# Kernel tuning notes

Measured on AMD Instinct MI355X. Metric: run time of the kernel, lower is better.

## Reference

```python
import jax, jax.numpy as jnp
import numpy as np

INPUT_SIZE = 8
HIDDEN = 12
N_ACTIONS = 4
B, T = 4096, 1024


def setup_inputs() -> dict:
    key = jax.random.key(0)
    ks = jax.random.split(key, 7)
    s_ih = 1.0 / np.sqrt(HIDDEN)
    # PyTorch LSTM params: W_ih [4H, I], W_hh [4H, H], b_ih [4H], b_hh [4H]; gate order i,f,g,o
    return {
        "x": jax.random.normal(ks[0], (B, T, INPUT_SIZE), dtype=jnp.float32),
        "W_ih": jax.random.uniform(ks[1], (4 * HIDDEN, INPUT_SIZE), jnp.float32, -s_ih, s_ih),
        "W_hh": jax.random.uniform(ks[2], (4 * HIDDEN, HIDDEN), jnp.float32, -s_ih, s_ih),
        "b_ih": jax.random.uniform(ks[3], (4 * HIDDEN,), jnp.float32, -s_ih, s_ih),
        "b_hh": jax.random.uniform(ks[4], (4 * HIDDEN,), jnp.float32, -s_ih, s_ih),
        "W_fc": jax.random.uniform(ks[5], (N_ACTIONS, HIDDEN), jnp.float32, -s_ih, s_ih),
        "b_fc": jax.random.uniform(ks[6], (N_ACTIONS,), jnp.float32, -s_ih, s_ih),
    }


def _lstm(x, W_ih, W_hh, b_ih, b_hh):
    # x: [B, T, I]. Precompute input contribution for all timesteps (one big GEMM).
    xW = jnp.einsum("bti,gi->tbg", x, W_ih) + (b_ih + b_hh)  # [T, B, 4H]
    Bsz = x.shape[0]
    h0 = jnp.zeros((Bsz, HIDDEN), x.dtype)
    c0 = jnp.zeros((Bsz, HIDDEN), x.dtype)

    def step(carry, xw_t):
        h, c = carry
        gates = xw_t + h @ W_hh.T  # [B, 4H]
        i, f, g, o = jnp.split(gates, 4, axis=-1)  # PyTorch gate order i,f,g,o
        i = jax.nn.sigmoid(i)
        f = jax.nn.sigmoid(f)
        g = jnp.tanh(g)
        o = jax.nn.sigmoid(o)
        c = f * c + i * g
        h = o * jnp.tanh(c)
        return (h, c), h

    (hn, cn), hs = jax.lax.scan(step, (h0, c0), xW)
    return jnp.swapaxes(hs, 0, 1), hn, cn  # hs -> [B, T, H]


def reference(x, W_ih, W_hh, b_ih, b_hh, W_fc, b_fc):
    hs, hn, cn = _lstm(x, W_ih, W_hh, b_ih, b_hh)
    out = hs @ W_fc.T + b_fc  # [B, T, n_actions]
    # match torch: hn/cn have leading num_layers dim (=1)
    return out, (hn[None], cn[None])
```

## Files before the change

### kernel.cpp

```cpp
#include <hip/hip_runtime.h>
#include <cstddef>
#include <cstdint>

namespace {

typedef __fp16 h2v __attribute__((ext_vector_type(2)));

constexpr int kB = 4096, kT = 1024, kI = 8, kH = 12, kA = 4;
constexpr int kTC = 32;
constexpr int kNCH = kT / kTC;
constexpr int kWaveU = 256;
constexpr int kBlkU  = 4 * kWaveU;

constexpr float kL2E  = 1.442695041f;
constexpr float kL2E2 = 2.885390082f;

template<int N>
__device__ __forceinline__ uint32_t ror16u(uint32_t v) {
    return (uint32_t)__builtin_amdgcn_mov_dpp((int)v, 0x120 + N, 0xF, 0xF, false);
}
__device__ __forceinline__ float ror16f1(float v) {
    return __int_as_float(__builtin_amdgcn_mov_dpp(__float_as_int(v), 0x121, 0xF, 0xF, false));
}
__device__ __forceinline__ float bperm(int byte_addr, float v) {
    return __int_as_float(__builtin_amdgcn_ds_bpermute(byte_addr, __float_as_int(v)));
}
__device__ __forceinline__ uint32_t pkrtz(float lo, float hi) {
    auto v = __builtin_amdgcn_cvt_pkrtz(lo, hi);
    return __builtin_bit_cast(uint32_t, v);
}
__device__ __forceinline__ h2v uh(uint32_t u) { return __builtin_bit_cast(h2v, u); }

__global__ __launch_bounds__(256, 2)
void lstm_fused_kernel(const float* __restrict__ x,
                       const float* __restrict__ W_ih,
                       const float* __restrict__ W_hh,
                       const float* __restrict__ b_ih,
                       const float* __restrict__ b_hh,
                       const float* __restrict__ W_fc,
                       const float* __restrict__ b_fc,
                       float* __restrict__ out) {
    __shared__ uint32_t xs[2][kBlkU];

    const int tid = threadIdx.x;
    const int wv  = tid >> 6;
    const int l64 = tid & 63;
    const int ri  = l64 >> 4;
    const int r   = l64 & 15;
    const int e   = ri & 1;
    const int gh  = ri >> 1;
    const int b0  = blockIdx.x * 8 + wv * 2;
    const int b   = b0 + e;
    const bool isFC = (gh == 0) && (r >= kH);
    const int a  = isFC ? (r - kH) : 0;

    const int probe = __builtin_amdgcn_mov_dpp(r, 0x121, 0xF, 0xF, false);
    const int dir   = (probe - r) & 15;

    h2v w1p[8], w2p[8], x1p[4], x2p[4];
    float b1, b2;
    if (r < kH) {
        const int row1 = (gh == 0) ? r : (2 * kH + r);
        const int row2 = (gh == 0) ? (kH + r) : (3 * kH + r);
        const float scl1 = (gh == 0) ? -kL2E : -kL2E2;
        const float scl2 = -kL2E;
#pragma unroll
        for (int j = 0; j < 8; ++j) {
            const int c0 = (r + dir * 2 * j) & 15;
            const int cc = (c0 + dir) & 15;
            const float u0 = (c0 < kH) ? W_hh[row1 * kH + c0] : 0.0f;
            const float u1 = (cc < kH) ? W_hh[row1 * kH + cc] : 0.0f;
            const float v0 = (c0 < kH) ? W_hh[row2 * kH + c0] : 0.0f;
            const float v1 = (cc < kH) ? W_hh[row2 * kH + cc] : 0.0f;
            w1p[j] = h2v{(__fp16)(scl1 * u0), (__fp16)(scl1 * u1)};
            w2p[j] = h2v{(__fp16)(scl2 * v0), (__fp16)(scl2 * v1)};
        }
#pragma unroll
        for (int i2 = 0; i2 < 4; ++i2) {
            x1p[i2] = h2v{(__fp16)(scl1 * W_ih[row1 * kI + 2 * i2]),
                          (__fp16)(scl1 * W_ih[row1 * kI + 2 * i2 + 1])};
            x2p[i2] = h2v{(__fp16)(scl2 * W_ih[row2 * kI + 2 * i2]),
                          (__fp16)(scl2 * W_ih[row2 * kI + 2 * i2 + 1])};
        }
        b1 = scl1 * (b_ih[row1] + b_hh[row1]);
        b2 = scl2 * (b_ih[row2] + b_hh[row2]);
    } else if (gh == 0) {
#pragma unroll
        for (int j = 0; j < 8; ++j) {
            const int c0 = (r + dir * 2 * j) & 15;
            const int cc = (c0 + dir) & 15;
            const float u0 = (c0 < kH) ? W_fc[a * kH + c0] : 0.0f;
            const float u1 = (cc < kH) ? W_fc[a * kH + cc] : 0.0f;
            w1p[j] = h2v{(__fp16)u0, (__fp16)u1};
            w2p[j] = h2v{(__fp16)0.f, (__fp16)0.f};
        }
#pragma unroll
        for (int i2 = 0; i2 < 4; ++i2) {
            x1p[i2] = h2v{(__fp16)0.f, (__fp16)0.f};
            x2p[i2] = h2v{(__fp16)0.f, (__fp16)0.f};
        }
        b1 = b_fc[a]; b2 = 0.0f;
    } else {
#pragma unroll
        for (int j = 0; j < 8; ++j) { w1p[j] = h2v{(__fp16)0.f, (__fp16)0.f}; w2p[j] = w1p[j]; }
#pragma unroll
        for (int i2 = 0; i2 < 4; ++i2) { x1p[i2] = h2v{(__fp16)0.f, (__fp16)0.f}; x2p[i2] = x1p[i2]; }
        b1 = 0.0f; b2 = 0.0f;
    }
    const float m1  = (gh == 0) ? 1.0f : 2.0f;
    const float a1c = (gh == 0) ? 0.0f : -1.0f;
    const int  exa  = (l64 ^ 32) << 2;

    const float* xga = x + (size_t)b0 * (kT * kI);
    const float* xgb = xga + (size_t)kT * kI;
    const int wbu = wv * kWaveU;
    const int rbu = wbu + e * 128;

    float4 rva = ((const float4*)xga)[l64];
    float4 rvb = ((const float4*)xgb)[l64];
    {
        uint2 ua; ua.x = pkrtz(rva.x, rva.y); ua.y = pkrtz(rva.z, rva.w);
        uint2 ub; ub.x = pkrtz(rvb.x, rvb.y); ub.y = pkrtz(rvb.z, rvb.w);
        *(uint2*)&xs[0][wbu + l64 * 2]       = ua;
        *(uint2*)&xs[0][wbu + 128 + l64 * 2] = ub;
    }
    asm volatile("s_waitcnt lgkmcnt(0)" ::: "memory");
    __builtin_amdgcn_sched_barrier(0);
    uint4 xr = *(const uint4*)&xs[0][rbu];

    float h = 0.0f, c = 0.0f;
    uint32_t hrp[8];
#pragma unroll
    for (int k = 0; k < 8; ++k) hrp[k] = 0u;

    float* op = out + (size_t)b * (kT * kA) + a;

    int cb = 0;
#pragma unroll 1
    for (int ch = 0; ch < kNCH; ++ch) {
        if (ch + 1 < kNCH) {
            rva = ((const float4*)(xga + (size_t)(ch + 1) * (kTC * kI)))[l64];
            rvb = ((const float4*)(xgb + (size_t)(ch + 1) * (kTC * kI)))[l64];
        }
#pragma unroll 2
        for (int tt = 0; tt < kTC; ++tt) {
            float s1 = b1, s2 = b2;
#pragma unroll
            for (int j = 0; j < 8; ++j) {
                const h2v hv = uh(hrp[j]);
                s1 = __builtin_amdgcn_fdot2(w1p[j], hv, s1, false);
                s2 = __builtin_amdgcn_fdot2(w2p[j], hv, s2, false);
            }
            s1 = __builtin_amdgcn_fdot2(x1p[0], uh(xr.x), s1, false);
            s2 = __builtin_amdgcn_fdot2(x2p[0], uh(xr.x), s2, false);
            s1 = __builtin_amdgcn_fdot2(x1p[1], uh(xr.y), s1, false);
            s2 = __builtin_amdgcn_fdot2(x2p[1], uh(xr.y), s2, false);
            s1 = __builtin_amdgcn_fdot2(x1p[2], uh(xr.z), s1, false);
            s2 = __builtin_amdgcn_fdot2(x2p[2], uh(xr.z), s2, false);
            s1 = __builtin_amdgcn_fdot2(x1p[3], uh(xr.w), s1, false);
            s2 = __builtin_amdgcn_fdot2(x2p[3], uh(xr.w), s2, false);
            if (tt + 1 < kTC) xr = *(const uint4*)&xs[cb][rbu + (tt + 1) * 4];
            if ((ch | tt) != 0) { if (isFC) op[-kA] = s1; }
            const float e1   = __builtin_amdgcn_exp2f(s1);
            const float act1 = fmaf(m1, __builtin_amdgcn_rcpf(1.0f + e1), a1c);
            const float e2   = __builtin_amdgcn_exp2f(s2);
            const float act2 = __builtin_amdgcn_rcpf(1.0f + e2);
            const float o1 = bperm(exa, act1);
            const float o2 = bperm(exa, act2);
            const float fv = (gh == 0) ? act2 : o2;
            const float ov = (gh == 0) ? o2 : act2;
            c = fmaf(fv, c, act1 * o1);
            const float ec = __builtin_amdgcn_exp2f(-kL2E2 * c);
            const float tc = fmaf(2.0f, __builtin_amdgcn_rcpf(1.0f + ec), -1.0f);
            h = ov * tc;
            const float hn1 = ror16f1(h);
            const uint32_t Q = pkrtz(h, hn1);
            hrp[0] = Q;
            hrp[1] = ror16u<2>(Q);
            hrp[2] = ror16u<4>(Q);
            hrp[3] = ror16u<6>(Q);
            hrp[4] = ror16u<8>(Q);
            hrp[5] = ror16u<10>(Q);
            hrp[6] = ror16u<12>(Q);
            hrp[7] = ror16u<14>(Q);
            op += kA;
        }
        if (ch + 1 < kNCH) {
            const int nb = cb ^ 1;
            uint2 ua; ua.x = pkrtz(rva.x, rva.y); ua.y = pkrtz(rva.z, rva.w);
            uint2 ub; ub.x = pkrtz(rvb.x, rvb.y); ub.y = pkrtz(rvb.z, rvb.w);
            *(uint2*)&xs[nb][wbu + l64 * 2]       = ua;
            *(uint2*)&xs[nb][wbu + 128 + l64 * 2] = ub;
            asm volatile("s_waitcnt lgkmcnt(0)" ::: "memory");
            __builtin_amdgcn_sched_barrier(0);
            xr = *(const uint4*)&xs[nb][rbu];
            cb = nb;
        }
    }

    {
        float s1 = b1;
#pragma unroll
        for (int j = 0; j < 8; ++j)
            s1 = __builtin_amdgcn_fdot2(w1p[j], uh(hrp[j]), s1, false);
        if (isFC) op[-kA] = s1;
    }
    if (gh == 0 && r < kH) {
        float* hn = out + (size_t)kB * kT * kA;
        hn[(size_t)b * kH + r] = h;
        hn[(size_t)kB * kH + (size_t)b * kH + r] = c;
    }
}

}

extern "C" void kernel_launch(void* const* d_in, const int* in_sizes, int n_in,
                              void* d_out, int out_size, void* d_ws, size_t ws_size,
                              hipStream_t stream) {
    (void)in_sizes; (void)n_in; (void)d_ws; (void)ws_size; (void)out_size;
    const float* x    = (const float*)d_in[0];
    const float* W_ih = (const float*)d_in[1];
    const float* W_hh = (const float*)d_in[2];
    const float* b_ih = (const float*)d_in[3];
    const float* b_hh = (const float*)d_in[4];
    const float* W_fc = (const float*)d_in[5];
    const float* b_fc = (const float*)d_in[6];
    float* out = (float*)d_out;
    hipLaunchKernelGGL(lstm_fused_kernel, dim3(kB / 8), dim3(256), 0, stream,
                       x, W_ih, W_hh, b_ih, b_hh, W_fc, b_fc, out);
}
```

Before: 298.2 us.

## Compute all four gates per lane, removing cross-lane bpermute exchange

Remaps work so each 16-lane group handles one batch element, and each lane computes all four LSTM gates for its hidden unit. This eliminates the per-step ds_bpermute exchange between half-waves on the recurrent critical path. The cost is twice the dot-product work per lane, half as many lanes in total, and fewer resident waves per CU (launch bounds lowered, 16 elements per block). The x-tile LDS load for the next step is also issued earlier to hide its latency.

Result: faster. 246.7 us (-17.3%).

```diff
diff --git a/kernel.cpp b/kernel.cpp
--- a/kernel.cpp
+++ b/kernel.cpp
@@ -7,10 +7,10 @@
 typedef __fp16 h2v __attribute__((ext_vector_type(2)));
 
 constexpr int kB = 4096, kT = 1024, kI = 8, kH = 12, kA = 4;
-constexpr int kTC = 32;
+constexpr int kTC  = 32;
 constexpr int kNCH = kT / kTC;
-constexpr int kWaveU = 256;
-constexpr int kBlkU  = 4 * kWaveU;
+constexpr int kXRegU = 132;
+constexpr int kBlkU  = 16 * kXRegU;
 
 constexpr float kL2E  = 1.442695041f;
 constexpr float kL2E2 = 2.885390082f;
@@ -22,16 +22,13 @@
 __device__ __forceinline__ float ror16f1(float v) {
     return __int_as_float(__builtin_amdgcn_mov_dpp(__float_as_int(v), 0x121, 0xF, 0xF, false));
 }
-__device__ __forceinline__ float bperm(int byte_addr, float v) {
-    return __int_as_float(__builtin_amdgcn_ds_bpermute(byte_addr, __float_as_int(v)));
-}
 __device__ __forceinline__ uint32_t pkrtz(float lo, float hi) {
     auto v = __builtin_amdgcn_cvt_pkrtz(lo, hi);
     return __builtin_bit_cast(uint32_t, v);
 }
 __device__ __forceinline__ h2v uh(uint32_t u) { return __builtin_bit_cast(h2v, u); }
 
-__global__ __launch_bounds__(256, 2)
+__global__ __launch_bounds__(256, 1)
 void lstm_fused_kernel(const float* __restrict__ x,
                        const float* __restrict__ W_ih,
                        const float* __restrict__ W_hh,
@@ -45,88 +42,77 @@
     const int tid = threadIdx.x;
     const int wv  = tid >> 6;
     const int l64 = tid & 63;
-    const int ri  = l64 >> 4;
+    const int grp = l64 >> 4;
     const int r   = l64 & 15;
-    const int e   = ri & 1;
-    const int gh  = ri >> 1;
-    const int b0  = blockIdx.x * 8 + wv * 2;
-    const int b   = b0 + e;
-    const bool isFC = (gh == 0) && (r >= kH);
-    const int a  = isFC ? (r - kH) : 0;
+    const int ei  = wv * 4 + grp;
+    const int b   = blockIdx.x * 16 + ei;
+    const bool isFC = (r >= kH);
+    const int a   = isFC ? (r - kH) : 0;
 
     const int probe = __builtin_amdgcn_mov_dpp(r, 0x121, 0xF, 0xF, false);
     const int dir   = (probe - r) & 15;
 
-    h2v w1p[8], w2p[8], x1p[4], x2p[4];
-    float b1, b2;
-    if (r < kH) {
-        const int row1 = (gh == 0) ? r : (2 * kH + r);
-        const int row2 = (gh == 0) ? (kH + r) : (3 * kH + r);
-        const float scl1 = (gh == 0) ? -kL2E : -kL2E2;
-        const float scl2 = -kL2E;
-#pragma unroll
-        for (int j = 0; j < 8; ++j) {
-            const int c0 = (r + dir * 2 * j) & 15;
-            const int cc = (c0 + dir) & 15;
-            const float u0 = (c0 < kH) ? W_hh[row1 * kH + c0] : 0.0f;
-            const float u1 = (cc < kH) ? W_hh[row1 * kH + cc] : 0.0f;
-            const float v0 = (c0 < kH) ? W_hh[row2 * kH + c0] : 0.0f;
-            const float v1 = (cc < kH) ? W_hh[row2 * kH + cc] : 0.0f;
-            w1p[j] = h2v{(__fp16)(scl1 * u0), (__fp16)(scl1 * u1)};
-            w2p[j] = h2v{(__fp16)(scl2 * v0), (__fp16)(scl2 * v1)};
+    h2v wp[4][8], xp[4][4];
+    float bs[4];
+    if (!isFC) {
+#pragma unroll
+        for (int g = 0; g < 4; ++g) {
+            const int row = g * kH + r;
+            const float scl = (g == 2) ? -kL2E2 : -kL2E;
+#pragma unroll
+            for (int jj = 0; jj < 8; ++jj) {
+                const int c0 = (r + dir * 2 * jj) & 15;
+                const int c1 = (c0 + dir) & 15;
+                const float u0 = (c0 < kH) ? W_hh[row * kH + c0] : 0.0f;
+                const float u1 = (c1 < kH) ? W_hh[row * kH + c1] : 0.0f;
+                wp[g][jj] = h2v{(__fp16)(scl * u0), (__fp16)(scl * u1)};
+            }
+#pragma unroll
+            for (int i2 = 0; i2 < 4; ++i2)
+                xp[g][i2] = h2v{(__fp16)(scl * W_ih[row * kI + 2 * i2]),
+                                (__fp16)(scl * W_ih[row * kI + 2 * i2 + 1])};
+            bs[g] = scl * (b_ih[row] + b_hh[row]);
+        }
+    } else {
+#pragma unroll
+        for (int jj = 0; jj < 8; ++jj) {
+            const int c0 = (r + dir * 2 * jj) & 15;
+            const int c1 = (c0 + dir) & 15;
+            const float u0 = (c0 < kH) ? W_fc[a * kH + c0] : 0.0f;
+            const float u1 = (c1 < kH) ? W_fc[a * kH + c1] : 0.0f;
+            wp[0][jj] = h2v{(__fp16)u0, (__fp16)u1};
+            wp[1][jj] = h2v{(__fp16)0.f, (__fp16)0.f};
+            wp[2][jj] = wp[1][jj];
+            wp[3][jj] = wp[1][jj];
         }
 #pragma unroll
         for (int i2 = 0; i2 < 4; ++i2) {
-            x1p[i2] = h2v{(__fp16)(scl1 * W_ih[row1 * kI + 2 * i2]),
-                          (__fp16)(scl1 * W_ih[row1 * kI + 2 * i2 + 1])};
-            x2p[i2] = h2v{(__fp16)(scl2 * W_ih[row2 * kI + 2 * i2]),
-                          (__fp16)(scl2 * W_ih[row2 * kI + 2 * i2 + 1])};
-        }
-        b1 = scl1 * (b_ih[row1] + b_hh[row1]);
-        b2 = scl2 * (b_ih[row2] + b_hh[row2]);
-    } else if (gh == 0) {
-#pragma unroll
-        for (int j = 0; j < 8; ++j) {
-            const int c0 = (r + dir * 2 * j) & 15;
-            const int cc = (c0 + dir) & 15;
-            const float u0 = (c0 < kH) ? W_fc[a * kH + c0] : 0.0f;
-            const float u1 = (cc < kH) ? W_fc[a * kH + cc] : 0.0f;
-            w1p[j] = h2v{(__fp16)u0, (__fp16)u1};
-            w2p[j] = h2v{(__fp16)0.f, (__fp16)0.f};
-        }
-#pragma unroll
-        for (int i2 = 0; i2 < 4; ++i2) {
-            x1p[i2] = h2v{(__fp16)0.f, (__fp16)0.f};
-            x2p[i2] = h2v{(__fp16)0.f, (__fp16)0.f};
-        }
-        b1 = b_fc[a]; b2 = 0.0f;
-    } else {
-#pragma unroll
-        for (int j = 0; j < 8; ++j) { w1p[j] = h2v{(__fp16)0.f, (__fp16)0.f}; w2p[j] = w1p[j]; }
-#pragma unroll
-        for (int i2 = 0; i2 < 4; ++i2) { x1p[i2] = h2v{(__fp16)0.f, (__fp16)0.f}; x2p[i2] = x1p[i2]; }
-        b1 = 0.0f; b2 = 0.0f;
-    }
-    const float m1  = (gh == 0) ? 1.0f : 2.0f;
-    const float a1c = (gh == 0) ? 0.0f : -1.0f;
-    const int  exa  = (l64 ^ 32) << 2;
-
-    const float* xga = x + (size_t)b0 * (kT * kI);
-    const float* xgb = xga + (size_t)kT * kI;
-    const int wbu = wv * kWaveU;
-    const int rbu = wbu + e * 128;
-
-    float4 rva = ((const float4*)xga)[l64];
-    float4 rvb = ((const float4*)xgb)[l64];
+            xp[0][i2] = h2v{(__fp16)0.f, (__fp16)0.f};
+            xp[1][i2] = xp[0][i2]; xp[2][i2] = xp[0][i2]; xp[3][i2] = xp[0][i2];
+        }
+        bs[0] = b_fc[a]; bs[1] = 0.0f; bs[2] = 0.0f; bs[3] = 0.0f;
+    }
+
+    const float* xg = x + (size_t)b * (kT * kI);
+    const int reg = ei * kXRegU;
+
+    float4 rv0, rv1, rv2, rv3;
     {
-        uint2 ua; ua.x = pkrtz(rva.x, rva.y); ua.y = pkrtz(rva.z, rva.w);
-        uint2 ub; ub.x = pkrtz(rvb.x, rvb.y); ub.y = pkrtz(rvb.z, rvb.w);
-        *(uint2*)&xs[0][wbu + l64 * 2]       = ua;
-        *(uint2*)&xs[0][wbu + 128 + l64 * 2] = ub;
+        const float4* gp = (const float4*)xg;
+        rv0 = gp[r]; rv1 = gp[16 + r]; rv2 = gp[32 + r]; rv3 = gp[48 + r];
+        uint2 u;
+        u.x = pkrtz(rv0.x, rv0.y); u.y = pkrtz(rv0.z, rv0.w);
+        *(uint2*)&xs[0][reg + 2 * r] = u;
+        u.x = pkrtz(rv1.x, rv1.y); u.y = pkrtz(rv1.z, rv1.w);
+        *(uint2*)&xs[0][reg + 32 + 2 * r] = u;
+        u.x = pkrtz(rv2.x, rv2.y); u.y = pkrtz(rv2.z, rv2.w);
+        *(uint2*)&xs[0][reg + 64 + 2 * r] = u;
+        u.x = pkrtz(rv3.x, rv3.y); u.y = pkrtz(rv3.z, rv3.w);
+        *(uint2*)&xs[0][reg + 96 + 2 * r] = u;
     }
     asm volatile("s_waitcnt lgkmcnt(0)" ::: "memory");
     __builtin_amdgcn_sched_barrier(0);
-    uint4 xr = *(const uint4*)&xs[0][rbu];
+    uint4 xr = *(const uint4*)&xs[0][reg];
 
     float h = 0.0f, c = 0.0f;
     uint32_t hrp[8];
@@ -139,37 +125,47 @@
 #pragma unroll 1
     for (int ch = 0; ch < kNCH; ++ch) {
         if (ch + 1 < kNCH) {
-            rva = ((const float4*)(xga + (size_t)(ch + 1) * (kTC * kI)))[l64];
-            rvb = ((const float4*)(xgb + (size_t)(ch + 1) * (kTC * kI)))[l64];
+            const float4* gp = (const float4*)(xg + (size_t)(ch + 1) * (kTC * kI));
+            rv0 = gp[r]; rv1 = gp[16 + r]; rv2 = gp[32 + r]; rv3 = gp[48 + r];
         }
 #pragma unroll 2
         for (int tt = 0; tt < kTC; ++tt) {
-            float s1 = b1, s2 = b2;
-#pragma unroll
-            for (int j = 0; j < 8; ++j) {
-                const h2v hv = uh(hrp[j]);
-                s1 = __builtin_amdgcn_fdot2(w1p[j], hv, s1, false);
-                s2 = __builtin_amdgcn_fdot2(w2p[j], hv, s2, false);
+            uint4 xrn;
+            if (tt + 1 < kTC) xrn = *(const uint4*)&xs[cb][reg + (tt + 1) * 4];
+            float s0 = bs[0], s1 = bs[1], s2 = bs[2], s3 = bs[3];
+#pragma unroll
+            for (int jj = 0; jj < 8; ++jj) {
+                const h2v hv = uh(hrp[jj]);
+                s0 = __builtin_amdgcn_fdot2(wp[0][jj], hv, s0, false);
+                s1 = __builtin_amdgcn_fdot2(wp[1][jj], hv, s1, false);
+                s2 = __builtin_amdgcn_fdot2(wp[2][jj], hv, s2, false);
+                s3 = __builtin_amdgcn_fdot2(wp[3][jj], hv, s3, false);
             }
-            s1 = __builtin_amdgcn_fdot2(x1p[0], uh(xr.x), s1, false);
-            s2 = __builtin_amdgcn_fdot2(x2p[0], uh(xr.x), s2, false);
-            s1 = __builtin_amdgcn_fdot2(x1p[1], uh(xr.y), s1, false);
-            s2 = __builtin_amdgcn_fdot2(x2p[1], uh(xr.y), s2, false);
-            s1 = __builtin_amdgcn_fdot2(x1p[2], uh(xr.z), s1, false);
-            s2 = __builtin_amdgcn_fdot2(x2p[2], uh(xr.z), s2, false);
-            s1 = __builtin_amdgcn_fdot2(x1p[3], uh(xr.w), s1, false);
-            s2 = __builtin_amdgcn_fdot2(x2p[3], uh(xr.w), s2, false);
-            if (tt + 1 < kTC) xr = *(const uint4*)&xs[cb][rbu + (tt + 1) * 4];
-            if ((ch | tt) != 0) { if (isFC) op[-kA] = s1; }
-            const float e1   = __builtin_amdgcn_exp2f(s1);
-            const float act1 = fmaf(m1, __builtin_amdgcn_rcpf(1.0f + e1), a1c);
-            const float e2   = __builtin_amdgcn_exp2f(s2);
-            const float act2 = __builtin_amdgcn_rcpf(1.0f + e2);
-            const float o1 = bperm(exa, act1);
-            const float o2 = bperm(exa, act2);
-            const float fv = (gh == 0) ? act2 : o2;
-            const float ov = (gh == 0) ? o2 : act2;
-            c = fmaf(fv, c, act1 * o1);
+            {
+                const h2v xv0 = uh(xr.x), xv1 = uh(xr.y), xv2 = uh(xr.z), xv3 = uh(xr.w);
+                s0 = __builtin_amdgcn_fdot2(xp[0][0], xv0, s0, false);
+                s1 = __builtin_amdgcn_fdot2(xp[1][0], xv0, s1, false);
+                s2 = __builtin_amdgcn_fdot2(xp[2][0], xv0, s2, false);
+                s3 = __builtin_amdgcn_fdot2(xp[3][0], xv0, s3, false);
+                s0 = __builtin_amdgcn_fdot2(xp[0][1], xv1, s0, false);
+                s1 = __builtin_amdgcn_fdot2(xp[1][1], xv1, s1, false);
+                s2 = __builtin_amdgcn_fdot2(xp[2][1], xv1, s2, false);
+                s3 = __builtin_amdgcn_fdot2(xp[3][1], xv1, s3, false);
+                s0 = __builtin_amdgcn_fdot2(xp[0][2], xv2, s0, false);
+                s1 = __builtin_amdgcn_fdot2(xp[1][2], xv2, s1, false);
+                s2 = __builtin_amdgcn_fdot2(xp[2][2], xv2, s2, false);
+                s3 = __builtin_amdgcn_fdot2(xp[3][2], xv2, s3, false);
+                s0 = __builtin_amdgcn_fdot2(xp[0][3], xv3, s0, false);
+                s1 = __builtin_amdgcn_fdot2(xp[1][3], xv3, s1, false);
+                s2 = __builtin_amdgcn_fdot2(xp[2][3], xv3, s2, false);
+                s3 = __builtin_amdgcn_fdot2(xp[3][3], xv3, s3, false);
+            }
+            if ((ch | tt) != 0) { if (isFC) op[-kA] = s0; }
+            const float iv = __builtin_amdgcn_rcpf(1.0f + __builtin_amdgcn_exp2f(s0));
+            const float fv = __builtin_amdgcn_rcpf(1.0f + __builtin_amdgcn_exp2f(s1));
+            const float gv = fmaf(2.0f, __builtin_amdgcn_rcpf(1.0f + __builtin_amdgcn_exp2f(s2)), -1.0f);
+            const float ov = __builtin_amdgcn_rcpf(1.0f + __builtin_amdgcn_exp2f(s3));
+            c = fmaf(fv, c, iv * gv);
             const float ec = __builtin_amdgcn_exp2f(-kL2E2 * c);
             const float tc = fmaf(2.0f, __builtin_amdgcn_rcpf(1.0f + ec), -1.0f);
             h = ov * tc;
@@ -183,29 +179,35 @@
             hrp[5] = ror16u<10>(Q);
             hrp[6] = ror16u<12>(Q);
             hrp[7] = ror16u<14>(Q);
+            if (tt + 1 < kTC) xr = xrn;
             op += kA;
         }
         if (ch + 1 < kNCH) {
             const int nb = cb ^ 1;
-            uint2 ua; ua.x = pkrtz(rva.x, rva.y); ua.y = pkrtz(rva.z, rva.w);
-            uint2 ub; ub.x = pkrtz(rvb.x, rvb.y); ub.y = pkrtz(rvb.z, rvb.w);
-            *(uint2*)&xs[nb][wbu + l64 * 2]       = ua;
-            *(uint2*)&xs[nb][wbu + 128 + l64 * 2] = ub;
+            uint2 u;
+            u.x = pkrtz(rv0.x, rv0.y); u.y = pkrtz(rv0.z, rv0.w);
+            *(uint2*)&xs[nb][reg + 2 * r] = u;
+            u.x = pkrtz(rv1.x, rv1.y); u.y = pkrtz(rv1.z, rv1.w);
+            *(uint2*)&xs[nb][reg + 32 + 2 * r] = u;
+            u.x = pkrtz(rv2.x, rv2.y); u.y = pkrtz(rv2.z, rv2.w);
+            *(uint2*)&xs[nb][reg + 64 + 2 * r] = u;
+            u.x = pkrtz(rv3.x, rv3.y); u.y = pkrtz(rv3.z, rv3.w);
+            *(uint2*)&xs[nb][reg + 96 + 2 * r] = u;
             asm volatile("s_waitcnt lgkmcnt(0)" ::: "memory");
             __builtin_amdgcn_sched_barrier(0);
-            xr = *(const uint4*)&xs[nb][rbu];
+            xr = *(const uint4*)&xs[nb][reg];
             cb = nb;
         }
     }
 
     {
-        float s1 = b1;
-#pragma unroll
-        for (int j = 0; j < 8; ++j)
-            s1 = __builtin_amdgcn_fdot2(w1p[j], uh(hrp[j]), s1, false);
-        if (isFC) op[-kA] = s1;
-    }
-    if (gh == 0 && r < kH) {
+        float s0 = bs[0];
+#pragma unroll
+        for (int jj = 0; jj < 8; ++jj)
+            s0 = __builtin_amdgcn_fdot2(wp[0][jj], uh(hrp[jj]), s0, false);
+        if (isFC) op[-kA] = s0;
+    }
+    if (!isFC) {
         float* hn = out + (size_t)kB * kT * kA;
         hn[(size_t)b * kH + r] = h;
         hn[(size_t)kB * kH + (size_t)b * kH + r] = c;
@@ -226,6 +228,6 @@
     const float* W_fc = (const float*)d_in[5];
     const float* b_fc = (const float*)d_in[6];
     float* out = (float*)d_out;
-    hipLaunchKernelGGL(lstm_fused_kernel, dim3(kB / 8), dim3(256), 0, stream,
+    hipLaunchKernelGGL(lstm_fused_kernel, dim3(kB / 16), dim3(256), 0, stream,
                        x, W_ih, W_hh, b_ih, b_hh, W_fc, b_fc, out);
 }
```
